# Optimization experiments

Hardware: AMD Instinct MI355X
Metric: run time of the kernel (lower is better)

Reference implementation:

```python
import jax, jax.numpy as jnp
import numpy as np

B, S, T, H, NH, NL = 16, 128, 64, 128, 8, 4
DH = H // NH
FF = 2 * H
SCALE = 1.0 / float(np.sqrt(DH))


def _ln(x, s, b):
    m = x.mean(-1, keepdims=True)
    v = ((x - m) ** 2).mean(-1, keepdims=True)
    return (x - m) * jax.lax.rsqrt(v + 1e-5) * s + b


def _block(x, mask, p):
    Wq, bq, Wk, bk, Wv, bv, Wo, bo, s1, c1, W1, d1, W2, d2, s2, c2 = p
    N, L, _ = x.shape
    q = (x @ Wq + bq).reshape(N, L, NH, DH)
    k = (x @ Wk + bk).reshape(N, L, NH, DH)
    v = (x @ Wv + bv).reshape(N, L, NH, DH)
    scores = jnp.einsum('nqhd,nkhd->nhqk', q, k) * SCALE
    scores = jnp.where(mask[:, None, :, :], scores, -1e9)
    a = jax.nn.softmax(scores, axis=-1)
    o = jnp.einsum('nhqk,nkhd->nqhd', a, v).reshape(N, L, H)
    x = _ln(x + o @ Wo + bo, s1, c1)
    h = jax.nn.relu(x @ W1 + d1)
    return _ln(x + h @ W2 + d2, s2, c2)


def setup_inputs():
    key = jax.random.key(0)
    ks = jax.random.split(key, 16)
    g = lambda k, shape: jax.random.normal(k, shape, jnp.float32) * 0.02
    return {
        'polylines': jax.random.normal(ks[0], (B, S, T, H), jnp.float32),
        'lengths': jax.random.randint(ks[1], (B, S), 0, T + 1),
        'proj_w': g(ks[2], (H, H)), 'proj_b': jnp.zeros((H,), jnp.float32),
        'proj_ln_s': jnp.ones((H,), jnp.float32), 'proj_ln_b': jnp.zeros((H,), jnp.float32),
        'pos_emb': g(ks[3], (1, T, H)),
        'Wq': g(ks[4], (NL, H, H)), 'bq': jnp.zeros((NL, H), jnp.float32),
        'Wk': g(ks[5], (NL, H, H)), 'bk': jnp.zeros((NL, H), jnp.float32),
        'Wv': g(ks[6], (NL, H, H)), 'bv': jnp.zeros((NL, H), jnp.float32),
        'Wo': g(ks[7], (NL, H, H)), 'bo': jnp.zeros((NL, H), jnp.float32),
        'ln1_s': jnp.ones((NL, H), jnp.float32), 'ln1_b': jnp.zeros((NL, H), jnp.float32),
        'W1': g(ks[8], (NL, H, FF)), 'b1': jnp.zeros((NL, FF), jnp.float32),
        'W2': g(ks[9], (NL, FF, H)), 'b2': jnp.zeros((NL, H), jnp.float32),
        'ln2_s': jnp.ones((NL, H), jnp.float32), 'ln2_b': jnp.zeros((NL, H), jnp.float32),
    }


def reference(polylines, lengths, proj_w, proj_b, proj_ln_s, proj_ln_b, pos_emb,
              Wq, bq, Wk, bk, Wv, bv, Wo, bo, ln1_s, ln1_b, W1, b1, W2, b2, ln2_s, ln2_b):
    # valid[b,s,t] = t < lengths[b,s]; lengths==0 -> polyline absent (fully padded)
    valid = jnp.arange(T)[None, None, :] < lengths[:, :, None]  # [B,S,T]
    x = jnp.where(valid[..., None], polylines, -1.0)            # -1 pad as in np.pad(constant_values=-1)
    # mask_temporal[b,s] = outer(valid[b,s], valid[b,s])
    mask_t = (valid[:, :, :, None] & valid[:, :, None, :]).reshape(B * S, T, T)
    # mask_spatial[b,t] = outer(valid[b,:,t], valid[b,:,t])
    vs = jnp.transpose(valid, (0, 2, 1))                        # [B,T,S]
    mask_s = (vs[:, :, :, None] & vs[:, :, None, :]).reshape(B * T, S, S)

    x = x.reshape(B * S, T, H)
    x = jax.nn.relu(_ln(x @ proj_w + proj_b, proj_ln_s, proj_ln_b))  # MLP: Linear->LN->ReLU
    x = x + pos_emb[:, :T, :]

    mask = mask_t
    for i in range(NL):
        if i == NL // 2:
            # switch from temporal to spatial attention: [B*S,T,H] -> [B*T,S,H]
            x = x.reshape(B, S, T, H).transpose(0, 2, 1, 3).reshape(B * T, S, H)
            mask = mask_s
        p = (Wq[i], bq[i], Wk[i], bk[i], Wv[i], bv[i], Wo[i], bo[i],
             ln1_s[i], ln1_b[i], W1[i], b1[i], W2[i], b2[i], ln2_s[i], ln2_b[i])
        x = _block(x, mask, p)
    # faithful to original final reshape (treats [B*T,S,H] buffer as [B,S,T,H])
    return x.reshape(B, S, T, H)[:, 0, :]
```

## Files before the change

### kernel.cpp

```cpp
#include <hip/hip_runtime.h>

typedef short short8 __attribute__((ext_vector_type(8)));
typedef short short4_t __attribute__((ext_vector_type(4)));
typedef float floatx4 __attribute__((ext_vector_type(4)));
typedef unsigned short ushort_t;

#define B_ 16
#define S_ 128
#define T_ 64
#define H_ 128
#define FF_ 256
#define SCALEQK 0.25f

#define OFFP 0
#define OFFQ(l) (16384 + (l) * 65536)
#define OFFK(l) (OFFQ(l) + 16384)
#define OFFV(l) (OFFQ(l) + 32768)
#define OFFO(l) (OFFQ(l) + 49152)
#define OFFW1(l) (278528 + (l) * 65536)
#define OFFW2(l) (OFFW1(l) + 32768)

__device__ __forceinline__ float b2f(ushort_t u) {
    union { unsigned int i; float f; } x; x.i = ((unsigned int)u) << 16; return x.f;
}
__device__ __forceinline__ ushort_t f2b(float f) {
    union { float f; unsigned int i; } x; x.f = f;
    unsigned int r = x.i + 0x7fffu + ((x.i >> 16) & 1u);
    return (ushort_t)(r >> 16);
}
__device__ __forceinline__ int pack2b(float a, float b) {
    return (int)f2b(a) | ((int)f2b(b) << 16);
}

struct WtEnt { const float* src; int N; int K; int nclog2; int dstoff; };
struct WtArgs { WtEnt e[25]; };

__global__ __launch_bounds__(256) void wt_kernel(WtArgs a, ushort_t* __restrict__ dst) {
    WtEnt ent = a.e[blockIdx.x];
    const int tiles_c = ent.N >> 5;
    const int nt = (ent.K >> 5) * tiles_c;
    const int t = blockIdx.y;
    if (t >= nt) return;
    const int tc = t & (tiles_c - 1);
    const int tr = t >> ent.nclog2;
    __shared__ float ld[32 * 33];
    const int tid = threadIdx.x;
#pragma unroll
    for (int i = 0; i < 4; ++i) {
        int e = tid + i * 256;
        int rr = e >> 5, cc = e & 31;
        ld[rr * 33 + cc] = ent.src[(tr * 32 + rr) * ent.N + tc * 32 + cc];
    }
    __syncthreads();
    ushort_t* d = dst + ent.dstoff;
#pragma unroll
    for (int i = 0; i < 4; ++i) {
        int e = tid + i * 256;
        int rr = e >> 5, cc = e & 31;
        d[(tc * 32 + rr) * ent.K + tr * 32 + cc] = f2b(ld[cc * 33 + rr]);
    }
}

template<int RT, int CT, int KK>
__device__ __forceinline__ void mm_g(const ushort_t* aL, int sa,
                                     const ushort_t* __restrict__ wT,
                                     int colbase, int lane, floatx4 (&acc)[RT][CT]) {
    const int l15 = lane & 15, lq8 = (lane >> 4) * 8;
#pragma unroll
    for (int r = 0; r < RT; ++r)
#pragma unroll
        for (int c = 0; c < CT; ++c) acc[r][c] = (floatx4){0.f, 0.f, 0.f, 0.f};
#pragma unroll
    for (int k0 = 0; k0 < KK; k0 += 32) {
        short8 b[CT];
#pragma unroll
        for (int c = 0; c < CT; ++c)
            b[c] = *(const short8*)&wT[(colbase + c * 16 + l15) * KK + k0 + lq8];
#pragma unroll
        for (int r = 0; r < RT; ++r) {
            short8 a = *(const short8*)&aL[(r * 16 + l15) * sa + k0 + lq8];
#pragma unroll
            for (int c = 0; c < CT; ++c)
                acc[r][c] = __builtin_amdgcn_mfma_f32_16x16x32_bf16(a, b[c], acc[r][c], 0, 0, 0);
        }
    }
}

template<int RT, int CT, int KK>
__device__ __forceinline__ void mm_g3(const ushort_t* aL, int sa,
                                      const ushort_t* __restrict__ w0,
                                      const ushort_t* __restrict__ w1,
                                      const ushort_t* __restrict__ w2,
                                      int colbase, int lane,
                                      floatx4 (&A0)[RT][CT], floatx4 (&A1)[RT][CT],
                                      floatx4 (&A2)[RT][CT]) {
    const int l15 = lane & 15, lq8 = (lane >> 4) * 8;
#pragma unroll
    for (int r = 0; r < RT; ++r)
#pragma unroll
        for (int c = 0; c < CT; ++c) {
            A0[r][c] = (floatx4){0.f, 0.f, 0.f, 0.f};
            A1[r][c] = (floatx4){0.f, 0.f, 0.f, 0.f};
            A2[r][c] = (floatx4){0.f, 0.f, 0.f, 0.f};
        }
#pragma unroll
    for (int k0 = 0; k0 < KK; k0 += 32) {
        short8 b0[CT], b1[CT], b2[CT];
#pragma unroll
        for (int c = 0; c < CT; ++c) {
            int co = (colbase + c * 16 + l15) * KK + k0 + lq8;
            b0[c] = *(const short8*)&w0[co];
            b1[c] = *(const short8*)&w1[co];
            b2[c] = *(const short8*)&w2[co];
        }
#pragma unroll
        for (int r = 0; r < RT; ++r) {
            short8 a = *(const short8*)&aL[(r * 16 + l15) * sa + k0 + lq8];
#pragma unroll
            for (int c = 0; c < CT; ++c) {
                A0[r][c] = __builtin_amdgcn_mfma_f32_16x16x32_bf16(a, b0[c], A0[r][c], 0, 0, 0);
                A1[r][c] = __builtin_amdgcn_mfma_f32_16x16x32_bf16(a, b1[c], A1[r][c], 0, 0, 0);
                A2[r][c] = __builtin_amdgcn_mfma_f32_16x16x32_bf16(a, b2[c], A2[r][c], 0, 0, 0);
            }
        }
    }
}

template<int RT, int CT, int KK>
__device__ __forceinline__ void mm_g2(const ushort_t* aL, int sa,
                                      const ushort_t* __restrict__ w0,
                                      const ushort_t* __restrict__ w1,
                                      int colbase, int lane,
                                      floatx4 (&A0)[RT][CT], floatx4 (&A1)[RT][CT]) {
    const int l15 = lane & 15, lq8 = (lane >> 4) * 8;
#pragma unroll
    for (int r = 0; r < RT; ++r)
#pragma unroll
        for (int c = 0; c < CT; ++c) {
            A0[r][c] = (floatx4){0.f, 0.f, 0.f, 0.f};
            A1[r][c] = (floatx4){0.f, 0.f, 0.f, 0.f};
        }
#pragma unroll
    for (int k0 = 0; k0 < KK; k0 += 32) {
        short8 b0[CT], b1[CT];
#pragma unroll
        for (int c = 0; c < CT; ++c) {
            int co = (colbase + c * 16 + l15) * KK + k0 + lq8;
            b0[c] = *(const short8*)&w0[co];
            b1[c] = *(const short8*)&w1[co];
        }
#pragma unroll
        for (int r = 0; r < RT; ++r) {
            short8 a = *(const short8*)&aL[(r * 16 + l15) * sa + k0 + lq8];
#pragma unroll
            for (int c = 0; c < CT; ++c) {
                A0[r][c] = __builtin_amdgcn_mfma_f32_16x16x32_bf16(a, b0[c], A0[r][c], 0, 0, 0);
                A1[r][c] = __builtin_amdgcn_mfma_f32_16x16x32_bf16(a, b1[c], A1[r][c], 0, 0, 0);
            }
        }
    }
}

template<int RT, int CT>
__device__ __forceinline__ void add_bias(floatx4 (&acc)[RT][CT], const float* b,
                                         int colbase, int l15) {
#pragma unroll
    for (int c = 0; c < CT; ++c) {
        float bc = b[colbase + c * 16 + l15];
#pragma unroll
        for (int r = 0; r < RT; ++r)
#pragma unroll
            for (int g = 0; g < 4; ++g) acc[r][c][g] += bc;
    }
}

template<int RT, int CT>
__device__ __forceinline__ void add_resid_reg(floatx4 (&acc)[RT][CT],
                                              const float (&res)[RT][CT][4]) {
#pragma unroll
    for (int r = 0; r < RT; ++r)
#pragma unroll
        for (int c = 0; c < CT; ++c)
#pragma unroll
            for (int g = 0; g < 4; ++g) acc[r][c][g] += res[r][c][g];
}
template<int RT, int CT>
__device__ __forceinline__ void save_resid(float (&res)[RT][CT][4],
                                           const floatx4 (&acc)[RT][CT]) {
#pragma unroll
    for (int r = 0; r < RT; ++r)
#pragma unroll
        for (int c = 0; c < CT; ++c)
#pragma unroll
            for (int g = 0; g < 4; ++g) res[r][c][g] = acc[r][c][g];
}

template<int RT, int CT>
__device__ __forceinline__ void st_n(const floatx4 (&acc)[RT][CT], ushort_t* dst, int stride,
                                     int colbase, int l15, int lq) {
#pragma unroll
    for (int r = 0; r < RT; ++r)
#pragma unroll
        for (int g = 0; g < 4; ++g) {
            int row = r * 16 + lq * 4 + g;
#pragma unroll
            for (int c = 0; c < CT; ++c)
                dst[row * stride + colbase + c * 16 + l15] = f2b(acc[r][c][g]);
        }
}

template<int RT, int CT>
__device__ __forceinline__ void st_t(const floatx4 (&acc)[RT][CT], ushort_t* dst, int stride,
                                     int colbase, int l15, int lq) {
#pragma unroll
    for (int r = 0; r < RT; ++r)
#pragma unroll
        for (int c = 0; c < CT; ++c) {
            int d = colbase + c * 16 + l15;
            short4_t p;
#pragma unroll
            for (int g = 0; g < 4; ++g) p[g] = (short)f2b(acc[r][c][g]);
            *(short4_t*)&dst[d * stride + r * 16 + lq * 4] = p;
        }
}

template<int RT, int CT>
__device__ __forceinline__ void ln_norm(floatx4 (&acc)[RT][CT], float* redL,
                                        const float* lns, const float* lnb,
                                        int colbase, int l15, int lq, int wv) {
#pragma unroll
    for (int r = 0; r < RT; ++r)
#pragma unroll
        for (int g = 0; g < 4; ++g) {
            float s = 0.f, q = 0.f;
#pragma unroll
            for (int c = 0; c < CT; ++c) { float v = acc[r][c][g]; s += v; q += v * v; }
            s += __shfl_xor(s, 1); s += __shfl_xor(s, 2); s += __shfl_xor(s, 4); s += __shfl_xor(s, 8);
            q += __shfl_xor(q, 1); q += __shfl_xor(q, 2); q += __shfl_xor(q, 4); q += __shfl_xor(q, 8);
            if (l15 == 0) {
                int row = r * 16 + lq * 4 + g;
                redL[row * 8 + wv] = s;
                redL[row * 8 + 4 + wv] = q;
            }
        }
    __syncthreads();
#pragma unroll
    for (int r = 0; r < RT; ++r)
#pragma unroll
        for (int g = 0; g < 4; ++g) {
            int row = r * 16 + lq * 4 + g;
            float4 S = *(float4*)&redL[row * 8];
            float4 Q = *(float4*)&redL[row * 8 + 4];
            float mean = (S.x + S.y + S.z + S.w) * (1.f / 128.f);
            float var = (Q.x + Q.y + Q.z + Q.w) * (1.f / 128.f) - mean * mean;
            float rstd = rsqrtf(var + 1e-5f);
#pragma unroll
            for (int c = 0; c < CT; ++c) {
                int col = colbase + c * 16 + l15;
                acc[r][c][g] = (acc[r][c][g] - mean) * rstd * lns[col] + lnb[col];
            }
        }
}

template<int JT>
__device__ __forceinline__ void softmax_pack(floatx4 (&st)[JT], bool iv, unsigned jm,
                                             int (&px)[JT][2]) {
    float ev[JT][4];
    float mx = -3.0e38f;
#pragma unroll
    for (int jt = 0; jt < JT; ++jt)
#pragma unroll
        for (int g = 0; g < 4; ++g) {
            bool ok = iv && ((jm >> (jt * 4 + g)) & 1u);
            float s = ok ? st[jt][g] * SCALEQK : -1e9f;
            ev[jt][g] = s; mx = fmaxf(mx, s);
        }
    mx = fmaxf(mx, __shfl_xor(mx, 16)); mx = fmaxf(mx, __shfl_xor(mx, 32));
    float sum = 0.f;
#pragma unroll
    for (int jt = 0; jt < JT; ++jt)
#pragma unroll
        for (int g = 0; g < 4; ++g) { float e = __expf(ev[jt][g] - mx); ev[jt][g] = e; sum += e; }
    sum += __shfl_xor(sum, 16); sum += __shfl_xor(sum, 32);
    float inv = 1.f / sum;
#pragma unroll
    for (int jt = 0; jt < JT; ++jt) {
        px[jt][0] = pack2b(ev[jt][0] * inv, ev[jt][1] * inv);
        px[jt][1] = pack2b(ev[jt][2] * inv, ev[jt][3] * inv);
    }
}

__device__ __forceinline__ short8 pfrag(const int (*px)[2], int jc, int lq, int l15) {
    const int jA = (lq & 1) * 32 + l15;
    int a0 = __shfl(px[jc * 2][0], jA);
    int a1 = __shfl(px[jc * 2][1], jA);
    int a2 = __shfl(px[jc * 2][0], jA + 16);
    int a3 = __shfl(px[jc * 2][1], jA + 16);
    int b0 = __shfl(px[jc * 2 + 1][0], jA);
    int b1 = __shfl(px[jc * 2 + 1][1], jA);
    int b2 = __shfl(px[jc * 2 + 1][0], jA + 16);
    int b3 = __shfl(px[jc * 2 + 1][1], jA + 16);
    const bool t = (lq >> 1) != 0;
    union { int4 i; short8 s; } u;
    u.i = make_int4(t ? b0 : a0, t ? b1 : a1, t ? b2 : a2, t ? b3 : a3);
    return u.s;
}
__device__ __forceinline__ short8 vfrag(const ushort_t* vT, int stride, int row, int off) {
    int2 a = *(const int2*)&vT[row * stride + off];
    int2 b = *(const int2*)&vT[row * stride + off + 4];
    union { int4 i; short8 s; } u;
    u.i = make_int4(a.x, a.y, b.x, b.y);
    return u.s;
}

__global__ __launch_bounds__(256, 2) void k1_mega(
    const float* __restrict__ poly, const int* __restrict__ lens,
    const ushort_t* __restrict__ wt,
    const float* __restrict__ projb, const float* __restrict__ pls,
    const float* __restrict__ plb, const float* __restrict__ pos,
    const float* __restrict__ bq0, const float* __restrict__ bk0,
    const float* __restrict__ bv0, const float* __restrict__ bo0,
    const float* __restrict__ l1s0, const float* __restrict__ l1b0,
    const float* __restrict__ b10, const float* __restrict__ b20,
    const float* __restrict__ l2s0, const float* __restrict__ l2b0,
    const float* __restrict__ bq1, const float* __restrict__ bk1,
    const float* __restrict__ bv1,
    ushort_t* __restrict__ o1, float* __restrict__ xr0f)
{
    __shared__ ushort_t pool[34816];
    __shared__ float redL[512];
    __shared__ float psL[8 * 68];
    __shared__ float q1L[128];
    ushort_t* xL = pool;
    ushort_t* qL = pool + 8704;
    ushort_t* kL = pool + 17408;
    ushort_t* vT = pool + 26112;
    ushort_t* hL = pool + 17408;

    const int tid = threadIdx.x, lane = tid & 63, wv = tid >> 6;
    const int l15 = lane & 15, lq = lane >> 4;
    const int gid = blockIdx.x;
    const int len = lens[gid];

    {
        const float* pg = poly + (size_t)gid * 8192;
#pragma unroll
        for (int it = 0; it < 8; ++it) {
            int e4 = (tid + it * 256) * 4;
            int row = e4 >> 7, col = e4 & 127;
            float4 f = *(const float4*)(pg + e4);
            if (row >= len) { f.x = -1.f; f.y = -1.f; f.z = -1.f; f.w = -1.f; }
            short4_t u;
            u[0] = (short)f2b(f.x); u[1] = (short)f2b(f.y);
            u[2] = (short)f2b(f.z); u[3] = (short)f2b(f.w);
            *(short4_t*)&xL[row * 136 + col] = u;
        }
    }
    __syncthreads();

    floatx4 a2[4][2];
    float xre[4][2][4];

    mm_g<4, 2, 128>(xL, 136, wt + OFFP, wv * 32, lane, a2);
    add_bias<4, 2>(a2, projb, wv * 32, l15);
    ln_norm<4, 2>(a2, redL, pls, plb, wv * 32, l15, lq, wv);
    __syncthreads();
#pragma unroll
    for (int r = 0; r < 4; ++r)
#pragma unroll
        for (int gg = 0; gg < 4; ++gg) {
            int row = r * 16 + lq * 4 + gg;
#pragma unroll
            for (int c = 0; c < 2; ++c) {
                int col = wv * 32 + c * 16 + l15;
                float v = fmaxf(a2[r][c][gg], 0.f) + pos[row * 128 + col];
                xre[r][c][gg] = v;
                xL[row * 136 + col] = f2b(v);
            }
        }
    __syncthreads();

    {
        floatx4 aq[4][2], ak[4][2], av[4][2];
        mm_g3<4, 2, 128>(xL, 136, wt + OFFQ(0), wt + OFFK(0), wt + OFFV(0),
                         wv * 32, lane, aq, ak, av);
        add_bias<4, 2>(aq, bq0, wv * 32, l15);
        st_n<4, 2>(aq, qL, 136, wv * 32, l15, lq);
        add_bias<4, 2>(ak, bk0, wv * 32, l15);
        st_n<4, 2>(ak, kL, 136, wv * 32, l15, lq);
        add_bias<4, 2>(av, bv0, wv * 32, l15);
        st_t<4, 2>(av, vT, 68, wv * 32, l15, lq);
    }
    __syncthreads();

    {
        const int iRow = wv * 16 + l15;
        const bool iv = iRow < len;
        unsigned jm = 0;
#pragma unroll
        for (int jt = 0; jt < 4; ++jt)
#pragma unroll
            for (int gg = 0; gg < 4; ++gg)
                if (jt * 16 + lq * 4 + gg < len) jm |= (1u << (jt * 4 + gg));
        for (int h = 0; h < 8; ++h) {
            const int hc = h * 16;
            short8 z8 = {0, 0, 0, 0, 0, 0, 0, 0};
            short8 bqf = z8;
            if (lq < 2) bqf = *(const short8*)&qL[iRow * 136 + hc + lq * 8];
            floatx4 st[4];
#pragma unroll
            for (int jt = 0; jt < 4; ++jt) {
                short8 ak = z8;
                if (lq < 2) ak = *(const short8*)&kL[(jt * 16 + l15) * 136 + hc + lq * 8];
                floatx4 zz = {0.f, 0.f, 0.f, 0.f};
                st[jt] = __builtin_amdgcn_mfma_f32_16x16x32_bf16(ak, bqf, zz, 0, 0, 0);
            }
            int px[4][2];
            softmax_pack<4>(st, iv, jm, px);
            floatx4 ao = {0.f, 0.f, 0.f, 0.f};
#pragma unroll
            for (int jc = 0; jc < 2; ++jc) {
                short8 av = vfrag(vT, 68, hc + l15, jc * 32 + lq * 8);
                short8 bp = pfrag(px, jc, lq, l15);
                ao = __builtin_amdgcn_mfma_f32_16x16x32_bf16(av, bp, ao, 0, 0, 0);
            }
            short4_t w;
#pragma unroll
            for (int gg = 0; gg < 4; ++gg) w[gg] = (short)f2b(ao[gg]);
            *(short4_t*)&qL[iRow * 136 + hc + lq * 4] = w;
        }
    }
    __syncthreads();

    mm_g<4, 2, 128>(qL, 136, wt + OFFO(0), wv * 32, lane, a2);
    add_bias<4, 2>(a2, bo0, wv * 32, l15);
    add_resid_reg<4, 2>(a2, xre);
    ln_norm<4, 2>(a2, redL, l1s0, l1b0, wv * 32, l15, lq, wv);
    save_resid<4, 2>(xre, a2);
    st_n<4, 2>(a2, xL, 136, wv * 32, l15, lq);
    __syncthreads();

    {
        floatx4 a4[4][4];
        mm_g<4, 4, 128>(xL, 136, wt + OFFW1(0), wv * 64, lane, a4);
        add_bias<4, 4>(a4, b10, wv * 64, l15);
#pragma unroll
        for (int r = 0; r < 4; ++r)
#pragma unroll
            for (int c = 0; c < 4; ++c)
#pragma unroll
                for (int gg = 0; gg < 4; ++gg) a4[r][c][gg] = fmaxf(a4[r][c][gg], 0.f);
        st_n<4, 4>(a4, hL, 272, wv * 64, l15, lq);
    }
    __syncthreads();

    mm_g<4, 2, 256>(hL, 272, wt + OFFW2(0), wv * 32, lane, a2);
    add_bias<4, 2>(a2, b20, wv * 32, l15);
    add_resid_reg<4, 2>(a2, xre);
    ln_norm<4, 2>(a2, redL, l2s0, l2b0, wv * 32, l15, lq, wv);
    save_resid<4, 2>(xre, a2);
    st_n<4, 2>(a2, xL, 136, wv * 32, l15, lq);
    if (lq == 0) {
#pragma unroll
        for (int c = 0; c < 2; ++c)
            xr0f[(size_t)gid * 128 + wv * 32 + c * 16 + l15] = a2[0][c][0];
    }
    __syncthreads();

    {
        floatx4 ak[4][2], av[4][2];
        mm_g2<4, 2, 128>(xL, 136, wt + OFFK(1), wt + OFFV(1), wv * 32, lane, ak, av);
        add_bias<4, 2>(ak, bk1, wv * 32, l15);
        st_n<4, 2>(ak, kL, 136, wv * 32, l15, lq);
        add_bias<4, 2>(av, bv1, wv * 32, l15);
        st_t<4, 2>(av, vT, 68, wv * 32, l15, lq);
    }
    if (tid < 128) {
        int d = tid;
        float a = bq1[d];
        const ushort_t* wq = wt + OFFQ(1) + d * 128;
#pragma unroll 4
        for (int j0 = 0; j0 < 128; j0 += 8) {
            short8 w8 = *(const short8*)&wq[j0];
            short8 x8 = *(const short8*)&xL[j0];
#pragma unroll
            for (int q = 0; q < 8; ++q)
                a = fmaf(b2f((ushort_t)x8[q]), b2f((ushort_t)w8[q]), a);
        }
        q1L[d] = a;
    }
    __syncthreads();

    {
        int h = tid >> 5, jj = tid & 31;
        int hc = h * 16;
        float s[2];
#pragma unroll
        for (int half = 0; half < 2; ++half) {
            int j = jj + half * 32;
            float a = 0.f;
            short8 k0v = *(const short8*)&kL[j * 136 + hc];
            short8 k1v = *(const short8*)&kL[j * 136 + hc + 8];
#pragma unroll
            for (int q = 0; q < 8; ++q) {
                a = fmaf(q1L[hc + q], b2f((ushort_t)k0v[q]), a);
                a = fmaf(q1L[hc + 8 + q], b2f((ushort_t)k1v[q]), a);
            }
            s[half] = (j < len) ? a * SCALEQK : -1e9f;
        }
        float mx = fmaxf(s[0], s[1]);
#pragma unroll
        for (int d = 1; d < 32; d <<= 1) mx = fmaxf(mx, __shfl_xor(mx, d));
        float e0 = __expf(s[0] - mx), e1 = __expf(s[1] - mx);
        float sum = e0 + e1;
#pragma unroll
        for (int d = 1; d < 32; d <<= 1) sum += __shfl_xor(sum, d);
        float inv = 1.f / sum;
        psL[h * 68 + jj] = e0 * inv;
        psL[h * 68 + jj + 32] = e1 * inv;
    }
    __syncthreads();
    if (tid < 128) {
        int h = tid >> 4, d = tid & 15, hc = h * 16;
        float a = 0.f;
#pragma unroll 4
        for (int j0 = 0; j0 < 64; j0 += 4) {
            float4 p4 = *(const float4*)&psL[h * 68 + j0];
            short4_t v4 = *(const short4_t*)&vT[(hc + d) * 68 + j0];
            a += p4.x * b2f((ushort_t)v4[0]) + p4.y * b2f((ushort_t)v4[1])
               + p4.z * b2f((ushort_t)v4[2]) + p4.w * b2f((ushort_t)v4[3]);
        }
        o1[(size_t)gid * 128 + hc + d] = f2b(a);
    }
}

__device__ __forceinline__ void k2a_body(char* smem, int blk,
    const ushort_t* __restrict__ xg, const int* __restrict__ lens,
    const ushort_t* __restrict__ wt, int l,
    const float* __restrict__ bq, const float* __restrict__ bk,
    const float* __restrict__ bv,
    ushort_t* __restrict__ aob)
{
    ushort_t* xL = (ushort_t*)(smem);
    ushort_t* qL = (ushort_t*)(smem + 34816);
    ushort_t* kL = (ushort_t*)(smem + 40960);
    ushort_t* vT = (ushort_t*)(smem + 47104);
    int* vldL = (int*)(smem + 51456);

    const int tid = threadIdx.x, lane = tid & 63, wv = tid >> 6;
    const int l15 = lane & 15, lq = lane >> 4;
    const int g = blk >> 3, h = blk & 7, hc = h * 16;
    const size_t rowg = (size_t)g * 128;

#pragma unroll
    for (int it = 0; it < 8; ++it) {
        int e8 = tid + it * 256;
        int row = e8 >> 4, kg = e8 & 15;
        *(short8*)&xL[row * 136 + kg * 8] = *(const short8*)&xg[(rowg + row) * 128 + kg * 8];
    }
    if (tid < 128) vldL[tid] = (lens[g * 128 + tid] > 0) ? 1 : 0;
    __syncthreads();

    unsigned jm = 0;
#pragma unroll
    for (int jt = 0; jt < 8; ++jt)
#pragma unroll
        for (int gg = 0; gg < 4; ++gg)
            if (vldL[jt * 16 + lq * 4 + gg]) jm |= (1u << (jt * 4 + gg));

    {
        floatx4 aq[2][1], ak[2][1], av[2][1];
        mm_g3<2, 1, 128>(xL + (wv * 32) * 136, 136, wt + OFFQ(l), wt + OFFK(l),
                         wt + OFFV(l), hc, lane, aq, ak, av);
        add_bias<2, 1>(aq, bq, hc, l15);
        st_n<2, 1>(aq, qL + (wv * 32) * 24, 24, 0, l15, lq);
        add_bias<2, 1>(ak, bk, hc, l15);
        st_n<2, 1>(ak, kL + (wv * 32) * 24, 24, 0, l15, lq);
        add_bias<2, 1>(av, bv, hc, l15);
        st_t<2, 1>(av, vT + wv * 32, 136, 0, l15, lq);
    }
    __syncthreads();

    for (int u = 0; u < 2; ++u) {
        const int iRow = wv * 32 + u * 16 + l15;
        const bool iv = vldL[iRow] != 0;
        short8 z8 = {0, 0, 0, 0, 0, 0, 0, 0};
        short8 bqf = z8;
        if (lq < 2) bqf = *(const short8*)&qL[iRow * 24 + lq * 8];
        floatx4 st[8];
#pragma unroll
        for (int jt = 0; jt < 8; ++jt) {
            short8 ak = z8;
            if (lq < 2) ak = *(const short8*)&kL[(jt * 16 + l15) * 24 + lq * 8];
            floatx4 zz = {0.f, 0.f, 0.f, 0.f};
            st[jt] = __builtin_amdgcn_mfma_f32_16x16x32_bf16(ak, bqf, zz, 0, 0, 0);
        }
        int px[8][2];
        softmax_pack<8>(st, iv, jm, px);
        floatx4 ao = {0.f, 0.f, 0.f, 0.f};
#pragma unroll
        for (int jc = 0; jc < 4; ++jc) {
            short8 av = vfrag(vT, 136, l15, jc * 32 + lq * 8);
            short8 bp = pfrag(px, jc, lq, l15);
            ao = __builtin_amdgcn_mfma_f32_16x16x32_bf16(av, bp, ao, 0, 0, 0);
        }
        short4_t w;
#pragma unroll
        for (int gg = 0; gg < 4; ++gg) w[gg] = (short)f2b(ao[gg]);
        *(short4_t*)&aob[(rowg + iRow) * 128 + hc + lq * 4] = w;
    }
}

template<bool FINAL>
__device__ __forceinline__ void k2b_body(char* smem, int blk,
    const ushort_t* __restrict__ ain, float* __restrict__ xr,
    const ushort_t* __restrict__ wt, int l,
    const float* bo_l, const float* l1s_l, const float* l1b_l,
    const float* b1_l, const float* b2_l, const float* l2s_l, const float* l2b_l,
    ushort_t* __restrict__ xg, float* __restrict__ outp)
{
    ushort_t* aL = (ushort_t*)(smem);
    ushort_t* hL = (ushort_t*)(smem + 4352);
    float* redL = (float*)(smem + 13056);

    const int tid = threadIdx.x, lane = tid & 63, wv = tid >> 6;
    const int l15 = lane & 15, lq = lane >> 4;
    const size_t rowbase = FINAL ? ((size_t)(blk >> 2) * 128 + (blk & 3) * 16)
                                 : ((size_t)blk * 16);

    {
        int row = tid >> 4, kg = tid & 15;
        *(short8*)&aL[row * 136 + kg * 8] = *(const short8*)&ain[(rowbase + row) * 128 + kg * 8];
    }
    __syncthreads();

    floatx4 a2[1][2];
    float xre[1][2][4];

    mm_g<1, 2, 128>(aL, 136, wt + OFFO(l), wv * 32, lane, a2);
    add_bias<1, 2>(a2, bo_l, wv * 32, l15);
#pragma unroll
    for (int c = 0; c < 2; ++c)
#pragma unroll
        for (int gg = 0; gg < 4; ++gg)
            a2[0][c][gg] += xr[(rowbase + lq * 4 + gg) * 128 + wv * 32 + c * 16 + l15];
    ln_norm<1, 2>(a2, redL, l1s_l, l1b_l, wv * 32, l15, lq, wv);
    save_resid<1, 2>(xre, a2);
    st_n<1, 2>(a2, aL, 136, wv * 32, l15, lq);
    __syncthreads();

    {
        floatx4 a4[1][4];
        mm_g<1, 4, 128>(aL, 136, wt + OFFW1(l), wv * 64, lane, a4);
        add_bias<1, 4>(a4, b1_l, wv * 64, l15);
#pragma unroll
        for (int c = 0; c < 4; ++c)
#pragma unroll
            for (int gg = 0; gg < 4; ++gg) a4[0][c][gg] = fmaxf(a4[0][c][gg], 0.f);
        st_n<1, 4>(a4, hL, 272, wv * 64, l15, lq);
    }
    __syncthreads();

    mm_g<1, 2, 256>(hL, 272, wt + OFFW2(l), wv * 32, lane, a2);
    add_bias<1, 2>(a2, b2_l, wv * 32, l15);
    add_resid_reg<1, 2>(a2, xre);
    ln_norm<1, 2>(a2, redL, l2s_l, l2b_l, wv * 32, l15, lq, wv);

    if (FINAL) {
#pragma unroll
        for (int c = 0; c < 2; ++c)
#pragma unroll
            for (int gg = 0; gg < 4; ++gg) {
                int orow = (blk >> 2) * 64 + (blk & 3) * 16 + lq * 4 + gg;
                outp[(size_t)orow * 128 + wv * 32 + c * 16 + l15] = a2[0][c][gg];
            }
    } else {
#pragma unroll
        for (int c = 0; c < 2; ++c)
#pragma unroll
            for (int gg = 0; gg < 4; ++gg) {
                size_t grow = rowbase + lq * 4 + gg;
                int col = wv * 32 + c * 16 + l15;
                float v = a2[0][c][gg];
                xg[grow * 128 + col] = f2b(v);
                xr[grow * 128 + col] = v;
            }
    }
}

__device__ __forceinline__ void sync_group(unsigned* pf, int idx, unsigned target, int tid) {
    __syncthreads();
    if (tid == 0) {
        __threadfence();
        __hip_atomic_fetch_add(&pf[idx * 16], 1u, __ATOMIC_RELEASE,
                               __HIP_MEMORY_SCOPE_AGENT);
        while (__hip_atomic_load(&pf[idx * 16], __ATOMIC_ACQUIRE,
                                 __HIP_MEMORY_SCOPE_AGENT) < target)
            __builtin_amdgcn_s_sleep(8);
        __threadfence();
    }
    __syncthreads();
}

__global__ __launch_bounds__(256) void k3_tail(
    const ushort_t* __restrict__ o1buf, float* __restrict__ xrf,
    const int* __restrict__ lens, const ushort_t* __restrict__ wt,
    const float* __restrict__ bq, const float* __restrict__ bk,
    const float* __restrict__ bv, const float* __restrict__ bo,
    const float* __restrict__ l1s, const float* __restrict__ l1b,
    const float* __restrict__ b1, const float* __restrict__ b2,
    const float* __restrict__ l2s, const float* __restrict__ l2b,
    ushort_t* __restrict__ xg, ushort_t* __restrict__ aob,
    float* __restrict__ outp, unsigned* __restrict__ pf)
{
    __shared__ __align__(16) char smem[51968];
    const int t = (int)blockIdx.x;
    const int g = t >> 3, sub = t & 7;
    const int tid = threadIdx.x;

    k2b_body<false>(smem, t, o1buf, xrf, wt, 1,
                    bo + H_, l1s + H_, l1b + H_, b1 + FF_, b2 + H_, l2s + H_, l2b + H_,
                    xg, nullptr);
    sync_group(pf, g * 4 + 0, 8, tid);

    k2a_body(smem, t, xg, lens, wt, 2, bq + 2 * H_, bk + 2 * H_, bv + 2 * H_, aob);
    sync_group(pf, g * 4 + 1, 8, tid);

    k2b_body<false>(smem, t, aob, xrf, wt, 2,
                    bo + 2 * H_, l1s + 2 * H_, l1b + 2 * H_, b1 + 2 * FF_, b2 + 2 * H_,
                    l2s + 2 * H_, l2b + 2 * H_,
                    xg, nullptr);
    sync_group(pf, g * 4 + 2, 8, tid);

    k2a_body(smem, t, xg, lens, wt, 3, bq + 3 * H_, bk + 3 * H_, bv + 3 * H_, aob);
    sync_group(pf, g * 4 + 3, 8, tid);

    if (sub < 4)
        k2b_body<true>(smem, g * 4 + sub, aob, xrf, wt, 3,
                       bo + 3 * H_, l1s + 3 * H_, l1b + 3 * H_, b1 + 3 * FF_, b2 + 3 * H_,
                       l2s + 3 * H_, l2b + 3 * H_,
                       nullptr, outp);
}

extern "C" void kernel_launch(void* const* d_in, const int* in_sizes, int n_in,
                              void* d_out, int out_size, void* d_ws, size_t ws_size,
                              hipStream_t stream)
{
    const float* poly   = (const float*)d_in[0];
    const int*   lens   = (const int*)d_in[1];
    const float* proj_w = (const float*)d_in[2];
    const float* proj_b = (const float*)d_in[3];
    const float* pls    = (const float*)d_in[4];
    const float* plb    = (const float*)d_in[5];
    const float* pos    = (const float*)d_in[6];
    const float* Wq = (const float*)d_in[7];
    const float* bq = (const float*)d_in[8];
    const float* Wk = (const float*)d_in[9];
    const float* bk = (const float*)d_in[10];
    const float* Wv = (const float*)d_in[11];
    const float* bv = (const float*)d_in[12];
    const float* Wo = (const float*)d_in[13];
    const float* bo = (const float*)d_in[14];
    const float* l1s = (const float*)d_in[15];
    const float* l1b = (const float*)d_in[16];
    const float* W1 = (const float*)d_in[17];
    const float* b1 = (const float*)d_in[18];
    const float* W2 = (const float*)d_in[19];
    const float* b2 = (const float*)d_in[20];
    const float* l2s = (const float*)d_in[21];
    const float* l2b = (const float*)d_in[22];
    float* outp = (float*)d_out;

    char* base = (char*)d_ws;
    ushort_t* wt    = (ushort_t*)base;
    ushort_t* o1buf = (ushort_t*)(base + 1081344);
    float* xrf      = (float*)(base + 1605632);
    ushort_t* xgbuf = (ushort_t*)(base + 2654208);
    ushort_t* aob   = (ushort_t*)(base + 3178496);
    unsigned* pf    = (unsigned*)(base + 3702784);

    hipMemsetAsync(pf, 0, 64 * 64, stream);

    const int HH = H_ * H_, HF = H_ * FF_;
    WtArgs wa;
    wa.e[0] = {proj_w, 128, 128, 2, OFFP};
    for (int l = 0; l < 4; ++l) {
        wa.e[1 + l * 4 + 0] = {Wq + l * HH, 128, 128, 2, OFFQ(l)};
        wa.e[1 + l * 4 + 1] = {Wk + l * HH, 128, 128, 2, OFFK(l)};
        wa.e[1 + l * 4 + 2] = {Wv + l * HH, 128, 128, 2, OFFV(l)};
        wa.e[1 + l * 4 + 3] = {Wo + l * HH, 128, 128, 2, OFFO(l)};
    }
    for (int l = 0; l < 4; ++l) {
        wa.e[17 + l * 2 + 0] = {W1 + l * HF, 256, 128, 3, OFFW1(l)};
        wa.e[17 + l * 2 + 1] = {W2 + l * HF, 128, 256, 2, OFFW2(l)};
    }
    wt_kernel<<<dim3(25, 32), 256, 0, stream>>>(wa, wt);

    k1_mega<<<dim3(2048), 256, 0, stream>>>(
        poly, lens, wt,
        proj_b, pls, plb, pos,
        bq, bk, bv, bo, l1s, l1b, b1, b2, l2s, l2b,
        bq + H_, bk + H_, bv + H_,
        o1buf, xrf);

    k3_tail<<<dim3(128), 256, 0, stream>>>(
        o1buf, xrf, lens, wt,
        bq, bk, bv, bo, l1s, l1b, b1, b2, l2s, l2b,
        xgbuf, aob, outp, pf);
}
```

Before: 388.0 us.

## Fuse layer-0 and tail kernels with per-group producer counters

Merges the per-polyline first-layer kernel and the spatial-attention tail into one launch. Each block bumps a release atomic counter for its group of 128 polylines once its outputs are written. Blocks 0–127 then spin on their group's counter and go straight into the tail stages, reusing the same shared-memory pool. The aim is to remove the kernel boundary and let tail work for finished groups overlap with first-layer blocks still running. The cost is spin-waiting blocks that hold CU slots, and a reliance on low-index blocks being scheduled so that progress is guaranteed.

```diff
diff --git a/kernel.cpp b/kernel.cpp
--- a/kernel.cpp
+++ b/kernel.cpp
@@ -313,227 +313,6 @@
     return u.s;
 }
 
-__global__ __launch_bounds__(256, 2) void k1_mega(
-    const float* __restrict__ poly, const int* __restrict__ lens,
-    const ushort_t* __restrict__ wt,
-    const float* __restrict__ projb, const float* __restrict__ pls,
-    const float* __restrict__ plb, const float* __restrict__ pos,
-    const float* __restrict__ bq0, const float* __restrict__ bk0,
-    const float* __restrict__ bv0, const float* __restrict__ bo0,
-    const float* __restrict__ l1s0, const float* __restrict__ l1b0,
-    const float* __restrict__ b10, const float* __restrict__ b20,
-    const float* __restrict__ l2s0, const float* __restrict__ l2b0,
-    const float* __restrict__ bq1, const float* __restrict__ bk1,
-    const float* __restrict__ bv1,
-    ushort_t* __restrict__ o1, float* __restrict__ xr0f)
-{
-    __shared__ ushort_t pool[34816];
-    __shared__ float redL[512];
-    __shared__ float psL[8 * 68];
-    __shared__ float q1L[128];
-    ushort_t* xL = pool;
-    ushort_t* qL = pool + 8704;
-    ushort_t* kL = pool + 17408;
-    ushort_t* vT = pool + 26112;
-    ushort_t* hL = pool + 17408;
-
-    const int tid = threadIdx.x, lane = tid & 63, wv = tid >> 6;
-    const int l15 = lane & 15, lq = lane >> 4;
-    const int gid = blockIdx.x;
-    const int len = lens[gid];
-
-    {
-        const float* pg = poly + (size_t)gid * 8192;
-#pragma unroll
-        for (int it = 0; it < 8; ++it) {
-            int e4 = (tid + it * 256) * 4;
-            int row = e4 >> 7, col = e4 & 127;
-            float4 f = *(const float4*)(pg + e4);
-            if (row >= len) { f.x = -1.f; f.y = -1.f; f.z = -1.f; f.w = -1.f; }
-            short4_t u;
-            u[0] = (short)f2b(f.x); u[1] = (short)f2b(f.y);
-            u[2] = (short)f2b(f.z); u[3] = (short)f2b(f.w);
-            *(short4_t*)&xL[row * 136 + col] = u;
-        }
-    }
-    __syncthreads();
-
-    floatx4 a2[4][2];
-    float xre[4][2][4];
-
-    mm_g<4, 2, 128>(xL, 136, wt + OFFP, wv * 32, lane, a2);
-    add_bias<4, 2>(a2, projb, wv * 32, l15);
-    ln_norm<4, 2>(a2, redL, pls, plb, wv * 32, l15, lq, wv);
-    __syncthreads();
-#pragma unroll
-    for (int r = 0; r < 4; ++r)
-#pragma unroll
-        for (int gg = 0; gg < 4; ++gg) {
-            int row = r * 16 + lq * 4 + gg;
-#pragma unroll
-            for (int c = 0; c < 2; ++c) {
-                int col = wv * 32 + c * 16 + l15;
-                float v = fmaxf(a2[r][c][gg], 0.f) + pos[row * 128 + col];
-                xre[r][c][gg] = v;
-                xL[row * 136 + col] = f2b(v);
-            }
-        }
-    __syncthreads();
-
-    {
-        floatx4 aq[4][2], ak[4][2], av[4][2];
-        mm_g3<4, 2, 128>(xL, 136, wt + OFFQ(0), wt + OFFK(0), wt + OFFV(0),
-                         wv * 32, lane, aq, ak, av);
-        add_bias<4, 2>(aq, bq0, wv * 32, l15);
-        st_n<4, 2>(aq, qL, 136, wv * 32, l15, lq);
-        add_bias<4, 2>(ak, bk0, wv * 32, l15);
-        st_n<4, 2>(ak, kL, 136, wv * 32, l15, lq);
-        add_bias<4, 2>(av, bv0, wv * 32, l15);
-        st_t<4, 2>(av, vT, 68, wv * 32, l15, lq);
-    }
-    __syncthreads();
-
-    {
-        const int iRow = wv * 16 + l15;
-        const bool iv = iRow < len;
-        unsigned jm = 0;
-#pragma unroll
-        for (int jt = 0; jt < 4; ++jt)
-#pragma unroll
-            for (int gg = 0; gg < 4; ++gg)
-                if (jt * 16 + lq * 4 + gg < len) jm |= (1u << (jt * 4 + gg));
-        for (int h = 0; h < 8; ++h) {
-            const int hc = h * 16;
-            short8 z8 = {0, 0, 0, 0, 0, 0, 0, 0};
-            short8 bqf = z8;
-            if (lq < 2) bqf = *(const short8*)&qL[iRow * 136 + hc + lq * 8];
-            floatx4 st[4];
-#pragma unroll
-            for (int jt = 0; jt < 4; ++jt) {
-                short8 ak = z8;
-                if (lq < 2) ak = *(const short8*)&kL[(jt * 16 + l15) * 136 + hc + lq * 8];
-                floatx4 zz = {0.f, 0.f, 0.f, 0.f};
-                st[jt] = __builtin_amdgcn_mfma_f32_16x16x32_bf16(ak, bqf, zz, 0, 0, 0);
-            }
-            int px[4][2];
-            softmax_pack<4>(st, iv, jm, px);
-            floatx4 ao = {0.f, 0.f, 0.f, 0.f};
-#pragma unroll
-            for (int jc = 0; jc < 2; ++jc) {
-                short8 av = vfrag(vT, 68, hc + l15, jc * 32 + lq * 8);
-                short8 bp = pfrag(px, jc, lq, l15);
-                ao = __builtin_amdgcn_mfma_f32_16x16x32_bf16(av, bp, ao, 0, 0, 0);
-            }
-            short4_t w;
-#pragma unroll
-            for (int gg = 0; gg < 4; ++gg) w[gg] = (short)f2b(ao[gg]);
-            *(short4_t*)&qL[iRow * 136 + hc + lq * 4] = w;
-        }
-    }
-    __syncthreads();
-
-    mm_g<4, 2, 128>(qL, 136, wt + OFFO(0), wv * 32, lane, a2);
-    add_bias<4, 2>(a2, bo0, wv * 32, l15);
-    add_resid_reg<4, 2>(a2, xre);
-    ln_norm<4, 2>(a2, redL, l1s0, l1b0, wv * 32, l15, lq, wv);
-    save_resid<4, 2>(xre, a2);
-    st_n<4, 2>(a2, xL, 136, wv * 32, l15, lq);
-    __syncthreads();
-
-    {
-        floatx4 a4[4][4];
-        mm_g<4, 4, 128>(xL, 136, wt + OFFW1(0), wv * 64, lane, a4);
-        add_bias<4, 4>(a4, b10, wv * 64, l15);
-#pragma unroll
-        for (int r = 0; r < 4; ++r)
-#pragma unroll
-            for (int c = 0; c < 4; ++c)
-#pragma unroll
-                for (int gg = 0; gg < 4; ++gg) a4[r][c][gg] = fmaxf(a4[r][c][gg], 0.f);
-        st_n<4, 4>(a4, hL, 272, wv * 64, l15, lq);
-    }
-    __syncthreads();
-
-    mm_g<4, 2, 256>(hL, 272, wt + OFFW2(0), wv * 32, lane, a2);
-    add_bias<4, 2>(a2, b20, wv * 32, l15);
-    add_resid_reg<4, 2>(a2, xre);
-    ln_norm<4, 2>(a2, redL, l2s0, l2b0, wv * 32, l15, lq, wv);
-    save_resid<4, 2>(xre, a2);
-    st_n<4, 2>(a2, xL, 136, wv * 32, l15, lq);
-    if (lq == 0) {
-#pragma unroll
-        for (int c = 0; c < 2; ++c)
-            xr0f[(size_t)gid * 128 + wv * 32 + c * 16 + l15] = a2[0][c][0];
-    }
-    __syncthreads();
-
-    {
-        floatx4 ak[4][2], av[4][2];
-        mm_g2<4, 2, 128>(xL, 136, wt + OFFK(1), wt + OFFV(1), wv * 32, lane, ak, av);
-        add_bias<4, 2>(ak, bk1, wv * 32, l15);
-        st_n<4, 2>(ak, kL, 136, wv * 32, l15, lq);
-        add_bias<4, 2>(av, bv1, wv * 32, l15);
-        st_t<4, 2>(av, vT, 68, wv * 32, l15, lq);
-    }
-    if (tid < 128) {
-        int d = tid;
-        float a = bq1[d];
-        const ushort_t* wq = wt + OFFQ(1) + d * 128;
-#pragma unroll 4
-        for (int j0 = 0; j0 < 128; j0 += 8) {
-            short8 w8 = *(const short8*)&wq[j0];
-            short8 x8 = *(const short8*)&xL[j0];
-#pragma unroll
-            for (int q = 0; q < 8; ++q)
-                a = fmaf(b2f((ushort_t)x8[q]), b2f((ushort_t)w8[q]), a);
-        }
-        q1L[d] = a;
-    }
-    __syncthreads();
-
-    {
-        int h = tid >> 5, jj = tid & 31;
-        int hc = h * 16;
-        float s[2];
-#pragma unroll
-        for (int half = 0; half < 2; ++half) {
-            int j = jj + half * 32;
-            float a = 0.f;
-            short8 k0v = *(const short8*)&kL[j * 136 + hc];
-            short8 k1v = *(const short8*)&kL[j * 136 + hc + 8];
-#pragma unroll
-            for (int q = 0; q < 8; ++q) {
-                a = fmaf(q1L[hc + q], b2f((ushort_t)k0v[q]), a);
-                a = fmaf(q1L[hc + 8 + q], b2f((ushort_t)k1v[q]), a);
-            }
-            s[half] = (j < len) ? a * SCALEQK : -1e9f;
-        }
-        float mx = fmaxf(s[0], s[1]);
-#pragma unroll
-        for (int d = 1; d < 32; d <<= 1) mx = fmaxf(mx, __shfl_xor(mx, d));
-        float e0 = __expf(s[0] - mx), e1 = __expf(s[1] - mx);
-        float sum = e0 + e1;
-#pragma unroll
-        for (int d = 1; d < 32; d <<= 1) sum += __shfl_xor(sum, d);
-        float inv = 1.f / sum;
-        psL[h * 68 + jj] = e0 * inv;
-        psL[h * 68 + jj + 32] = e1 * inv;
-    }
-    __syncthreads();
-    if (tid < 128) {
-        int h = tid >> 4, d = tid & 15, hc = h * 16;
-        float a = 0.f;
-#pragma unroll 4
-        for (int j0 = 0; j0 < 64; j0 += 4) {
-            float4 p4 = *(const float4*)&psL[h * 68 + j0];
-            short4_t v4 = *(const short4_t*)&vT[(hc + d) * 68 + j0];
-            a += p4.x * b2f((ushort_t)v4[0]) + p4.y * b2f((ushort_t)v4[1])
-               + p4.z * b2f((ushort_t)v4[2]) + p4.w * b2f((ushort_t)v4[3]);
-        }
-        o1[(size_t)gid * 128 + hc + d] = f2b(a);
-    }
-}
-
 __device__ __forceinline__ void k2a_body(char* smem, int blk,
     const ushort_t* __restrict__ xg, const int* __restrict__ lens,
     const ushort_t* __restrict__ wt, int l,
@@ -702,23 +481,249 @@
     __syncthreads();
 }
 
-__global__ __launch_bounds__(256) void k3_tail(
-    const ushort_t* __restrict__ o1buf, float* __restrict__ xrf,
-    const int* __restrict__ lens, const ushort_t* __restrict__ wt,
+__global__ __launch_bounds__(256, 2) void k_fused(
+    const float* __restrict__ poly, const int* __restrict__ lens,
+    const ushort_t* __restrict__ wt,
+    const float* __restrict__ projb, const float* __restrict__ pls,
+    const float* __restrict__ plb, const float* __restrict__ pos,
     const float* __restrict__ bq, const float* __restrict__ bk,
     const float* __restrict__ bv, const float* __restrict__ bo,
     const float* __restrict__ l1s, const float* __restrict__ l1b,
     const float* __restrict__ b1, const float* __restrict__ b2,
     const float* __restrict__ l2s, const float* __restrict__ l2b,
+    ushort_t* __restrict__ o1, float* __restrict__ xr0f,
     ushort_t* __restrict__ xg, ushort_t* __restrict__ aob,
-    float* __restrict__ outp, unsigned* __restrict__ pf)
+    float* __restrict__ outp,
+    unsigned* __restrict__ pf, unsigned* __restrict__ prod)
 {
-    __shared__ __align__(16) char smem[51968];
-    const int t = (int)blockIdx.x;
-    const int g = t >> 3, sub = t & 7;
-    const int tid = threadIdx.x;
-
-    k2b_body<false>(smem, t, o1buf, xrf, wt, 1,
+    __shared__ __align__(16) ushort_t pool[34816];
+    __shared__ float redL[512];
+    __shared__ float psL[8 * 68];
+    __shared__ float q1L[128];
+    ushort_t* xL = pool;
+    ushort_t* qL = pool + 8704;
+    ushort_t* kL = pool + 17408;
+    ushort_t* vT = pool + 26112;
+    ushort_t* hL = pool + 17408;
+
+    const int tid = threadIdx.x, lane = tid & 63, wv = tid >> 6;
+    const int l15 = lane & 15, lq = lane >> 4;
+    const int gid = blockIdx.x;
+    const int len = lens[gid];
+    const float* bq1 = bq + H_; const float* bk1 = bk + H_; const float* bv1 = bv + H_;
+
+    {
+        const float* pg = poly + (size_t)gid * 8192;
+#pragma unroll
+        for (int it = 0; it < 8; ++it) {
+            int e4 = (tid + it * 256) * 4;
+            int row = e4 >> 7, col = e4 & 127;
+            float4 f = *(const float4*)(pg + e4);
+            if (row >= len) { f.x = -1.f; f.y = -1.f; f.z = -1.f; f.w = -1.f; }
+            short4_t u;
+            u[0] = (short)f2b(f.x); u[1] = (short)f2b(f.y);
+            u[2] = (short)f2b(f.z); u[3] = (short)f2b(f.w);
+            *(short4_t*)&xL[row * 136 + col] = u;
+        }
+    }
+    __syncthreads();
+
+    floatx4 a2[4][2];
+    float xre[4][2][4];
+
+    mm_g<4, 2, 128>(xL, 136, wt + OFFP, wv * 32, lane, a2);
+    add_bias<4, 2>(a2, projb, wv * 32, l15);
+    ln_norm<4, 2>(a2, redL, pls, plb, wv * 32, l15, lq, wv);
+    __syncthreads();
+#pragma unroll
+    for (int r = 0; r < 4; ++r)
+#pragma unroll
+        for (int gg = 0; gg < 4; ++gg) {
+            int row = r * 16 + lq * 4 + gg;
+#pragma unroll
+            for (int c = 0; c < 2; ++c) {
+                int col = wv * 32 + c * 16 + l15;
+                float v = fmaxf(a2[r][c][gg], 0.f) + pos[row * 128 + col];
+                xre[r][c][gg] = v;
+                xL[row * 136 + col] = f2b(v);
+            }
+        }
+    __syncthreads();
+
+    {
+        floatx4 aq[4][2], ak[4][2], av[4][2];
+        mm_g3<4, 2, 128>(xL, 136, wt + OFFQ(0), wt + OFFK(0), wt + OFFV(0),
+                         wv * 32, lane, aq, ak, av);
+        add_bias<4, 2>(aq, bq, wv * 32, l15);
+        st_n<4, 2>(aq, qL, 136, wv * 32, l15, lq);
+        add_bias<4, 2>(ak, bk, wv * 32, l15);
+        st_n<4, 2>(ak, kL, 136, wv * 32, l15, lq);
+        add_bias<4, 2>(av, bv, wv * 32, l15);
+        st_t<4, 2>(av, vT, 68, wv * 32, l15, lq);
+    }
+    __syncthreads();
+
+    {
+        const int iRow = wv * 16 + l15;
+        const bool iv = iRow < len;
+        unsigned jm = 0;
+#pragma unroll
+        for (int jt = 0; jt < 4; ++jt)
+#pragma unroll
+            for (int gg = 0; gg < 4; ++gg)
+                if (jt * 16 + lq * 4 + gg < len) jm |= (1u << (jt * 4 + gg));
+        for (int h = 0; h < 8; ++h) {
+            const int hc = h * 16;
+            short8 z8 = {0, 0, 0, 0, 0, 0, 0, 0};
+            short8 bqf = z8;
+            if (lq < 2) bqf = *(const short8*)&qL[iRow * 136 + hc + lq * 8];
+            floatx4 st[4];
+#pragma unroll
+            for (int jt = 0; jt < 4; ++jt) {
+                short8 ak = z8;
+                if (lq < 2) ak = *(const short8*)&kL[(jt * 16 + l15) * 136 + hc + lq * 8];
+                floatx4 zz = {0.f, 0.f, 0.f, 0.f};
+                st[jt] = __builtin_amdgcn_mfma_f32_16x16x32_bf16(ak, bqf, zz, 0, 0, 0);
+            }
+            int px[4][2];
+            softmax_pack<4>(st, iv, jm, px);
+            floatx4 ao = {0.f, 0.f, 0.f, 0.f};
+#pragma unroll
+            for (int jc = 0; jc < 2; ++jc) {
+                short8 av = vfrag(vT, 68, hc + l15, jc * 32 + lq * 8);
+                short8 bp = pfrag(px, jc, lq, l15);
+                ao = __builtin_amdgcn_mfma_f32_16x16x32_bf16(av, bp, ao, 0, 0, 0);
+            }
+            short4_t w;
+#pragma unroll
+            for (int gg = 0; gg < 4; ++gg) w[gg] = (short)f2b(ao[gg]);
+            *(short4_t*)&qL[iRow * 136 + hc + lq * 4] = w;
+        }
+    }
+    __syncthreads();
+
+    mm_g<4, 2, 128>(qL, 136, wt + OFFO(0), wv * 32, lane, a2);
+    add_bias<4, 2>(a2, bo, wv * 32, l15);
+    add_resid_reg<4, 2>(a2, xre);
+    ln_norm<4, 2>(a2, redL, l1s, l1b, wv * 32, l15, lq, wv);
+    save_resid<4, 2>(xre, a2);
+    st_n<4, 2>(a2, xL, 136, wv * 32, l15, lq);
+    __syncthreads();
+
+    {
+        floatx4 a4[4][4];
+        mm_g<4, 4, 128>(xL, 136, wt + OFFW1(0), wv * 64, lane, a4);
+        add_bias<4, 4>(a4, b1, wv * 64, l15);
+#pragma unroll
+        for (int r = 0; r < 4; ++r)
+#pragma unroll
+            for (int c = 0; c < 4; ++c)
+#pragma unroll
+                for (int gg = 0; gg < 4; ++gg) a4[r][c][gg] = fmaxf(a4[r][c][gg], 0.f);
+        st_n<4, 4>(a4, hL, 272, wv * 64, l15, lq);
+    }
+    __syncthreads();
+
+    mm_g<4, 2, 256>(hL, 272, wt + OFFW2(0), wv * 32, lane, a2);
+    add_bias<4, 2>(a2, b2, wv * 32, l15);
+    add_resid_reg<4, 2>(a2, xre);
+    ln_norm<4, 2>(a2, redL, l2s, l2b, wv * 32, l15, lq, wv);
+    save_resid<4, 2>(xre, a2);
+    st_n<4, 2>(a2, xL, 136, wv * 32, l15, lq);
+    if (lq == 0) {
+#pragma unroll
+        for (int c = 0; c < 2; ++c)
+            xr0f[(size_t)gid * 128 + wv * 32 + c * 16 + l15] = a2[0][c][0];
+    }
+    __syncthreads();
+
+    {
+        floatx4 ak[4][2], av[4][2];
+        mm_g2<4, 2, 128>(xL, 136, wt + OFFK(1), wt + OFFV(1), wv * 32, lane, ak, av);
+        add_bias<4, 2>(ak, bk1, wv * 32, l15);
+        st_n<4, 2>(ak, kL, 136, wv * 32, l15, lq);
+        add_bias<4, 2>(av, bv1, wv * 32, l15);
+        st_t<4, 2>(av, vT, 68, wv * 32, l15, lq);
+    }
+    if (tid < 128) {
+        int d = tid;
+        float a = bq1[d];
+        const ushort_t* wq = wt + OFFQ(1) + d * 128;
+#pragma unroll 4
+        for (int j0 = 0; j0 < 128; j0 += 8) {
+            short8 w8 = *(const short8*)&wq[j0];
+            short8 x8 = *(const short8*)&xL[j0];
+#pragma unroll
+            for (int q = 0; q < 8; ++q)
+                a = fmaf(b2f((ushort_t)x8[q]), b2f((ushort_t)w8[q]), a);
+        }
+        q1L[d] = a;
+    }
+    __syncthreads();
+
+    {
+        int h = tid >> 5, jj = tid & 31;
+        int hc = h * 16;
+        float s[2];
+#pragma unroll
+        for (int half = 0; half < 2; ++half) {
+            int j = jj + half * 32;
+            float a = 0.f;
+            short8 k0v = *(const short8*)&kL[j * 136 + hc];
+            short8 k1v = *(const short8*)&kL[j * 136 + hc + 8];
+#pragma unroll
+            for (int q = 0; q < 8; ++q) {
+                a = fmaf(q1L[hc + q], b2f((ushort_t)k0v[q]), a);
+                a = fmaf(q1L[hc + 8 + q], b2f((ushort_t)k1v[q]), a);
+            }
+            s[half] = (j < len) ? a * SCALEQK : -1e9f;
+        }
+        float mx = fmaxf(s[0], s[1]);
+#pragma unroll
+        for (int d = 1; d < 32; d <<= 1) mx = fmaxf(mx, __shfl_xor(mx, d));
+        float e0 = __expf(s[0] - mx), e1 = __expf(s[1] - mx);
+        float sum = e0 + e1;
+#pragma unroll
+        for (int d = 1; d < 32; d <<= 1) sum += __shfl_xor(sum, d);
+        float inv = 1.f / sum;
+        psL[h * 68 + jj] = e0 * inv;
+        psL[h * 68 + jj + 32] = e1 * inv;
+    }
+    __syncthreads();
+    if (tid < 128) {
+        int h = tid >> 4, d = tid & 15, hc = h * 16;
+        float a = 0.f;
+#pragma unroll 4
+        for (int j0 = 0; j0 < 64; j0 += 4) {
+            float4 p4 = *(const float4*)&psL[h * 68 + j0];
+            short4_t v4 = *(const short4_t*)&vT[(hc + d) * 68 + j0];
+            a += p4.x * b2f((ushort_t)v4[0]) + p4.y * b2f((ushort_t)v4[1])
+               + p4.z * b2f((ushort_t)v4[2]) + p4.w * b2f((ushort_t)v4[3]);
+        }
+        o1[(size_t)gid * 128 + hc + d] = f2b(a);
+    }
+
+    __syncthreads();
+    if (tid == 0) {
+        __threadfence();
+        __hip_atomic_fetch_add(&prod[(gid >> 7) * 16], 1u, __ATOMIC_RELEASE,
+                               __HIP_MEMORY_SCOPE_AGENT);
+    }
+
+    if (gid >= 128) return;
+
+    const int t = gid, g = t >> 3, sub = t & 7;
+    char* smem = (char*)pool;
+
+    if (tid == 0) {
+        while (__hip_atomic_load(&prod[g * 16], __ATOMIC_ACQUIRE,
+                                 __HIP_MEMORY_SCOPE_AGENT) < 128u)
+            __builtin_amdgcn_s_sleep(8);
+        __threadfence();
+    }
+    __syncthreads();
+
+    k2b_body<false>(smem, t, o1, xr0f, wt, 1,
                     bo + H_, l1s + H_, l1b + H_, b1 + FF_, b2 + H_, l2s + H_, l2b + H_,
                     xg, nullptr);
     sync_group(pf, g * 4 + 0, 8, tid);
@@ -726,7 +731,7 @@
     k2a_body(smem, t, xg, lens, wt, 2, bq + 2 * H_, bk + 2 * H_, bv + 2 * H_, aob);
     sync_group(pf, g * 4 + 1, 8, tid);
 
-    k2b_body<false>(smem, t, aob, xrf, wt, 2,
+    k2b_body<false>(smem, t, aob, xr0f, wt, 2,
                     bo + 2 * H_, l1s + 2 * H_, l1b + 2 * H_, b1 + 2 * FF_, b2 + 2 * H_,
                     l2s + 2 * H_, l2b + 2 * H_,
                     xg, nullptr);
@@ -736,7 +741,7 @@
     sync_group(pf, g * 4 + 3, 8, tid);
 
     if (sub < 4)
-        k2b_body<true>(smem, g * 4 + sub, aob, xrf, wt, 3,
+        k2b_body<true>(smem, g * 4 + sub, aob, xr0f, wt, 3,
                        bo + 3 * H_, l1s + 3 * H_, l1b + 3 * H_, b1 + 3 * FF_, b2 + 3 * H_,
                        l2s + 3 * H_, l2b + 3 * H_,
                        nullptr, outp);
@@ -778,8 +783,9 @@
     ushort_t* xgbuf = (ushort_t*)(base + 2654208);
     ushort_t* aob   = (ushort_t*)(base + 3178496);
     unsigned* pf    = (unsigned*)(base + 3702784);
-
-    hipMemsetAsync(pf, 0, 64 * 64, stream);
+    unsigned* prod  = (unsigned*)(base + 3706880);
+
+    hipMemsetAsync(pf, 0, 4096 + 1024, stream);
 
     const int HH = H_ * H_, HF = H_ * FF_;
     WtArgs wa;
@@ -796,15 +802,9 @@
     }
     wt_kernel<<<dim3(25, 32), 256, 0, stream>>>(wa, wt);
 
-    k1_mega<<<dim3(2048), 256, 0, stream>>>(
+    k_fused<<<dim3(2048), 256, 0, stream>>>(
         poly, lens, wt,
         proj_b, pls, plb, pos,
         bq, bk, bv, bo, l1s, l1b, b1, b2, l2s, l2b,
-        bq + H_, bk + H_, bv + H_,
-        o1buf, xrf);
-
-    k3_tail<<<dim3(128), 256, 0, stream>>>(
-        o1buf, xrf, lens, wt,
-        bq, bk, bv, bo, l1s, l1b, b1, b2, l2s, l2b,
-        xgbuf, aob, outp, pf);
-}
+        o1buf, xrf, xgbuf, aob, outp, pf, prod);
+}
```

Result: slower. 601.6 us (+55.1%).
